# Performance work log

Measured on AMD Instinct MI355X. Metric: run time of the kernel, lower is better.

## Reference

```python
import jax, jax.numpy as jnp
import numpy as np

EPS = 0.97  # ContrastLoss eps
T = 0.07    # temperature

def _embed(x, W, b):
    # Linear + L2 normalize (Normalize(power=2))
    h = x @ W.T + b                     # [B, feat_dim]
    norm = jnp.sqrt(jnp.sum(h * h, axis=1, keepdims=True))
    return h / norm

def setup_inputs() -> dict:
    key = jax.random.key(0)
    ks = jax.random.split(key, 7)
    B, S, Td, F = 8192, 2048, 2048, 128
    return {
        "f_s": jax.random.normal(ks[0], (B, S), jnp.float32),
        "f_t": jax.random.normal(ks[1], (B, Td), jnp.float32),
        "y": jax.random.randint(ks[2], (B,), 0, 100, jnp.int64),
        "W_s": jax.random.normal(ks[3], (F, S), jnp.float32) * 0.02,
        "b_s": jax.random.normal(ks[4], (F,), jnp.float32) * 0.02,
        "W_t": jax.random.normal(ks[5], (F, Td), jnp.float32) * 0.02,
        "b_t": jax.random.normal(ks[6], (F,), jnp.float32) * 0.02,
    }

def reference(f_s, f_t, y, W_s, b_s, W_t, b_t):
    fs = _embed(f_s, W_s, b_s)
    ft = _embed(f_t, W_t, b_t)
    # CRDLoss re-normalizes (idempotent, kept for fidelity)
    fs = fs / jnp.linalg.norm(fs, axis=1, keepdims=True)
    ft = ft / jnp.linalg.norm(ft, axis=1, keepdims=True)
    bsz = fs.shape[0]
    x = jnp.exp((fs @ ft.T) / T)  # [B, B] exponentiated similarities
    same = y[None, :] == y[:, None]        # y_expand == y_expand.T
    diag = jnp.eye(bsz, dtype=bool)
    pos_mask = same & ~diag
    neg_mask = ~same & ~diag
    # masked log-ratio sums instead of dynamic-shape gathers
    log_D1 = jnp.log(x / (x + EPS))
    log_D0 = jnp.log(EPS / (x + EPS))
    loss = -(jnp.sum(jnp.where(pos_mask, log_D1, 0.0))
             + jnp.sum(jnp.where(neg_mask, log_D0, 0.0))) / bsz
    return loss
```

## Files before the change

kernel.cpp:

```cpp
#include <hip/hip_runtime.h>
#include <math.h>


typedef _Float16 half_t;
typedef half_t halfx4 __attribute__((ext_vector_type(4)));
typedef half_t halfx8 __attribute__((ext_vector_type(8)));
typedef float f32x4 __attribute__((ext_vector_type(4)));

#define B_TOT   8192
#define K_EMB   2048
#define F_DIM   128
#define INV_T   14.285714285714286f
#define EPS_C   0.97f
#define CU_L2   20.60992915555662f
#define LN2_D   0.6931471805599453
#define LNEPS_D (-0.030459207484708574)

__device__ __forceinline__ float fexp2(float x) {
#if __has_builtin(__builtin_amdgcn_exp2f)
    return __builtin_amdgcn_exp2f(x);
#else
    return __expf(x * 0.6931471805599453f);
#endif
}
__device__ __forceinline__ float flog2(float x) {
#if __has_builtin(__builtin_amdgcn_logf)
    return __builtin_amdgcn_logf(x);
#else
    return __logf(x) * 1.4426950408889634f;
#endif
}

__global__ __launch_bounds__(256) void cvt_w_kernel(
    const float* __restrict__ Ws, const float* __restrict__ Wt,
    half_t* __restrict__ Ws16, half_t* __restrict__ Wt16)
{
    const float* src = blockIdx.y ? Wt : Ws;
    half_t* dst = blockIdx.y ? Wt16 : Ws16;
    int pos4 = blockIdx.x * 256 + threadIdx.x;
    float4 v = *(const float4*)(src + (size_t)pos4 * 4);
    halfx4 h4 = {(half_t)v.x, (half_t)v.y, (half_t)v.z, (half_t)v.w};
    *(halfx4*)(dst + (size_t)pos4 * 4) = h4;
}

__device__ __forceinline__ void cvst(uint4* dst, float4 x, float4 y)
{
    halfx8 h = {(half_t)x.x, (half_t)x.y, (half_t)x.z, (half_t)x.w,
                (half_t)y.x, (half_t)y.y, (half_t)y.z, (half_t)y.w};
    *(halfx8*)dst = h;
}

__device__ __forceinline__ void gload_lds16(const void* g, void* l)
{
    __builtin_amdgcn_global_load_lds(
        (const __attribute__((address_space(1))) void*)g,
        (__attribute__((address_space(3))) void*)l,
        16, 0, 0);
}

__global__ __launch_bounds__(256) void embed_kernel(
    const float* __restrict__ Xs, const float* __restrict__ Xt,
    const half_t* __restrict__ Ws16, const half_t* __restrict__ Wt16,
    const float* __restrict__ bs, const float* __restrict__ bt,
    half_t* __restrict__ outs, half_t* __restrict__ outt)
{
    const float* X; const half_t* W16; const float* bias; half_t* out;
    if (blockIdx.y == 0) { X = Xs; W16 = Ws16; bias = bs; out = outs; }
    else                 { X = Xt; W16 = Wt16; bias = bt; out = outt; }

    __shared__ uint4 smem[5120];

    const int tid  = threadIdx.x;
    const int r0   = blockIdx.x * 32;
    const int lane = tid & 63;
    const int w    = tid >> 6;
    const int wm   = w & 1, wn = w >> 1;
    const int l16  = lane & 15, lhi = lane >> 4;

    float bv[4];
#pragma unroll
    for (int in = 0; in < 4; ++in) bv[in] = bias[wn * 64 + in * 16 + l16];

    const int ar0 = tid >> 4;
    const int ac  = tid & 15;
    const int axz = ac ^ ar0;
    const float* aptr0 = X + (size_t)(r0 + ar0) * K_EMB + ac * 8;
    const float* aptr1 = aptr0 + (size_t)16 * K_EMB;

    const half_t* bgp[8];
#pragma unroll
    for (int i = 0; i < 8; ++i) {
        int rl = w * 32 + i * 4 + (lane >> 4);
        bgp[i] = W16 + (size_t)rl * K_EMB + (size_t)(((lane & 15) ^ (rl & 15)) * 8);
    }

    f32x4 acc[4];
#pragma unroll
    for (int in = 0; in < 4; ++in) acc[in] = f32x4{0.f, 0.f, 0.f, 0.f};

    float4 aR[4];

#define LOADA(T) do {                                                          \
        aR[0] = *(const float4*)(aptr0 + (size_t)(T) * 128);                   \
        aR[1] = *(const float4*)(aptr0 + (size_t)(T) * 128 + 4);               \
        aR[2] = *(const float4*)(aptr1 + (size_t)(T) * 128);                   \
        aR[3] = *(const float4*)(aptr1 + (size_t)(T) * 128 + 4);               \
    } while (0)

#define CVTA(BUF) do {                                                         \
        cvst(&smem[(BUF) * 512 + ar0 * 16 + axz], aR[0], aR[1]);               \
        cvst(&smem[(BUF) * 512 + ar0 * 16 + 256 + axz], aR[2], aR[3]);         \
    } while (0)

#define BGLL(BUF, T) do {                                                      \
        _Pragma("unroll")                                                      \
        for (int i = 0; i < 8; ++i)                                            \
            gload_lds16(bgp[i] + (size_t)(T) * 128,                            \
                        &smem[1024 + (BUF) * 2048 + w * 512 + i * 64]);        \
    } while (0)

#define COMPUTE(BUF) do {                                                      \
        _Pragma("unroll")                                                      \
        for (int kk = 0; kk < 4; ++kk) {                                       \
            const int sl = (kk * 4 + lhi) ^ l16;                               \
            halfx8 afrag = *(const halfx8*)&smem[(BUF) * 512 +                 \
                                                 (wm * 16 + l16) * 16 + sl];   \
            _Pragma("unroll")                                                  \
            for (int in = 0; in < 4; ++in) {                                   \
                halfx8 bfrag = *(const halfx8*)&smem[1024 + (BUF) * 2048 +     \
                                     (wn * 64 + in * 16 + l16) * 16 + sl];     \
                acc[in] = __builtin_amdgcn_mfma_f32_16x16x32_f16(              \
                    afrag, bfrag, acc[in], 0, 0, 0);                           \
            }                                                                  \
        }                                                                      \
    } while (0)

    BGLL(0, 0);
    LOADA(0);
    CVTA(0);
    LOADA(1);
    BGLL(1, 1);
    asm volatile("s_waitcnt lgkmcnt(0)" ::: "memory");
    __builtin_amdgcn_s_barrier();

#pragma unroll 2
    for (int t = 0; t < 14; ++t) {
        const int buf = t & 1;
        COMPUTE(buf);
        CVTA(buf ^ 1);
        LOADA(t + 2);
        asm volatile("s_waitcnt vmcnt(4) lgkmcnt(0)" ::: "memory");
        __builtin_amdgcn_s_barrier();
        BGLL(buf, t + 2);
    }
    COMPUTE(0);
    CVTA(1);
    asm volatile("s_waitcnt vmcnt(0) lgkmcnt(0)" ::: "memory");
    __builtin_amdgcn_s_barrier();
    COMPUTE(1);

#undef LOADA
#undef CVTA
#undef BGLL
#undef COMPUTE

    float* redS = (float*)smem;
    float* invS = ((float*)smem) + 64;

    float hh[4][4];
    float psum[4];
#pragma unroll
    for (int reg = 0; reg < 4; ++reg) {
        float p = 0.f;
#pragma unroll
        for (int in = 0; in < 4; ++in) {
            float v = acc[in][reg] + bv[in];
            hh[in][reg] = v;
            p += v * v;
        }
        p += __shfl_xor(p, 1);
        p += __shfl_xor(p, 2);
        p += __shfl_xor(p, 4);
        p += __shfl_xor(p, 8);
        psum[reg] = p;
    }
    if (l16 == 0)
#pragma unroll
        for (int reg = 0; reg < 4; ++reg)
            redS[(wm * 16 + lhi * 4 + reg) * 2 + wn] = psum[reg];
    __syncthreads();
    if (tid < 32) invS[tid] = rsqrtf(redS[tid * 2] + redS[tid * 2 + 1]);
    __syncthreads();

#pragma unroll
    for (int in = 0; in < 4; ++in)
#pragma unroll
        for (int reg = 0; reg < 4; ++reg) {
            int row = wm * 16 + lhi * 4 + reg;
            int col = wn * 64 + in * 16 + l16;
            out[(size_t)(r0 + row) * F_DIM + col] = (half_t)(hh[in][reg] * invS[row]);
        }
}

__global__ __launch_bounds__(256) void loss_kernel(
    const half_t* __restrict__ FS, const half_t* __restrict__ FT,
    const int* __restrict__ y, double* __restrict__ partials)
{
    __shared__ uint4 As4[128 * 8];
    __shared__ uint4 Bs4[128 * 8];
    __shared__ int   yrl[128], ycl[128];
    __shared__ float wsum[4];

    const int tid = threadIdx.x;
    const int i0  = blockIdx.x * 128;
    const int j0  = blockIdx.y * 128;

    if (tid < 128) yrl[tid] = y[i0 + tid];
    else           ycl[tid - 128] = y[j0 + tid - 128];

    const int lane = tid & 63;
    const int w    = tid >> 6;
    const int wm   = w >> 1, wn = w & 1;
    const int l16  = lane & 15, lhi = lane >> 4;

#pragma unroll
    for (int i = 0; i < 4; ++i) {
        int f = tid + i * 256;
        int row = f >> 3, c = f & 7;
        As4[row * 8 + (c ^ (row & 7))] = *(const uint4*)(FS + (size_t)(i0 + row) * F_DIM + c * 8);
    }
#pragma unroll
    for (int i = 0; i < 4; ++i) {
        int f = tid + i * 256;
        int row = f >> 3, c = f & 7;
        Bs4[row * 8 + (c ^ (row & 7))] = *(const uint4*)(FT + (size_t)(j0 + row) * F_DIM + c * 8);
    }
    __syncthreads();

    f32x4 acc[4][4];
    for (int im = 0; im < 4; ++im)
        for (int in = 0; in < 4; ++in)
            acc[im][in] = f32x4{0.f, 0.f, 0.f, 0.f};

    for (int kc = 0; kc < 2; ++kc) {
#pragma unroll
        for (int kk = 0; kk < 2; ++kk) {
            halfx8 a[4], b[4];
#pragma unroll
            for (int im = 0; im < 4; ++im) {
                int r = wm * 64 + im * 16 + l16;
                a[im] = *(const halfx8*)&As4[r * 8 + ((kk * 4 + lhi) ^ (r & 7))];
            }
#pragma unroll
            for (int in = 0; in < 4; ++in) {
                int r = wn * 64 + in * 16 + l16;
                b[in] = *(const halfx8*)&Bs4[r * 8 + ((kk * 4 + lhi) ^ (r & 7))];
            }
#pragma unroll
            for (int im = 0; im < 4; ++im)
#pragma unroll
                for (int in = 0; in < 4; ++in)
                    acc[im][in] = __builtin_amdgcn_mfma_f32_16x16x32_f16(
                        a[im], b[in], acc[im][in], 0, 0, 0);
        }
        if (kc == 0) {
            __syncthreads();
#pragma unroll
            for (int i = 0; i < 4; ++i) {
                int f = tid + i * 256;
                int row = f >> 3, c = f & 7;
                As4[row * 8 + (c ^ (row & 7))] =
                    *(const uint4*)(FS + (size_t)(i0 + row) * F_DIM + 64 + c * 8);
            }
#pragma unroll
            for (int i = 0; i < 4; ++i) {
                int f = tid + i * 256;
                int row = f >> 3, c = f & 7;
                Bs4[row * 8 + (c ^ (row & 7))] =
                    *(const uint4*)(FT + (size_t)(j0 + row) * F_DIM + 64 + c * 8);
            }
            __syncthreads();
        }
    }

    int yclv[4];
#pragma unroll
    for (int in = 0; in < 4; ++in) yclv[in] = ycl[wn * 64 + in * 16 + l16];

    float sumL = 0.f, sumU = 0.f;
    if (i0 != j0) {
#pragma unroll
        for (int im = 0; im < 4; ++im)
#pragma unroll
            for (int reg = 0; reg < 4; ++reg) {
                const int yi = yrl[wm * 64 + im * 16 + lhi * 4 + reg];
#pragma unroll
                for (int in = 0; in < 4; ++in) {
                    float u  = acc[im][in][reg] * CU_L2;
                    float e  = fexp2(u);
                    float l2 = flog2(e + EPS_C);
                    sumL += l2;
                    sumU += (yi == yclv[in]) ? u : 0.f;
                }
            }
    } else {
#pragma unroll
        for (int im = 0; im < 4; ++im)
#pragma unroll
            for (int reg = 0; reg < 4; ++reg) {
                const int il = wm * 64 + im * 16 + lhi * 4 + reg;
                const int yi = yrl[il];
#pragma unroll
                for (int in = 0; in < 4; ++in) {
                    const int jl = wn * 64 + in * 16 + l16;
                    float u  = acc[im][in][reg] * CU_L2;
                    float e  = fexp2(u);
                    float l2 = flog2(e + EPS_C);
                    bool off = (il != jl);
                    sumL += off ? l2 : 0.f;
                    sumU += (off && yi == yclv[in]) ? u : 0.f;
                }
            }
    }

    float local = sumU - sumL;
    for (int m = 1; m < 64; m <<= 1) local += __shfl_xor(local, m);
    if (lane == 0) wsum[w] = local;
    __syncthreads();
    if (tid == 0)
        partials[blockIdx.y * gridDim.x + blockIdx.x] =
            ((double)wsum[0] + (double)wsum[1]) + ((double)wsum[2] + (double)wsum[3]);
}

__global__ __launch_bounds__(256) void finalize_kernel(
    const double* __restrict__ partials, const int* __restrict__ y,
    float* __restrict__ out)
{
    __shared__ double sh[4];
    __shared__ int hist[128];
    if (threadIdx.x < 128) hist[threadIdx.x] = 0;
    __syncthreads();
    for (int i = threadIdx.x; i < B_TOT; i += 256) atomicAdd(&hist[y[i]], 1);

    double loc = 0.0;
    for (int i = threadIdx.x; i < 4096; i += 256) loc += partials[i];
    for (int m = 1; m < 64; m <<= 1) loc += __shfl_xor(loc, m);
    int lane = threadIdx.x & 63, w = threadIdx.x >> 6;
    if (lane == 0) sh[w] = loc;
    __syncthreads();
    if (threadIdx.x == 0) {
        long long npos = 0;
        for (int c = 0; c < 128; ++c) {
            long long n = hist[c];
            npos += n * n;
        }
        npos -= B_TOT;
        long long nneg = (long long)B_TOT * (B_TOT - 1) - npos;
        double total = (sh[0] + sh[1]) + (sh[2] + sh[3]);
        out[0] = (float)(-(LN2_D * total + (double)nneg * LNEPS_D) / (double)B_TOT);
    }
}

extern "C" void kernel_launch(void* const* d_in, const int* in_sizes, int n_in,
                              void* d_out, int out_size, void* d_ws, size_t ws_size,
                              hipStream_t stream)
{
    const size_t WS_NEEDED = (64 << 10) + (4 << 20) + (1 << 20);
    if (ws_size < WS_NEEDED) return;

    const float* f_s = (const float*)d_in[0];
    const float* f_t = (const float*)d_in[1];
    const int*   y   = (const int*)d_in[2];
    const float* W_s = (const float*)d_in[3];
    const float* b_s = (const float*)d_in[4];
    const float* W_t = (const float*)d_in[5];
    const float* b_t = (const float*)d_in[6];
    float* out = (float*)d_out;

    char* ws = (char*)d_ws;
    double* partials = (double*)ws;
    half_t* fs   = (half_t*)(ws + (64 << 10));
    half_t* ft   = (half_t*)(ws + (64 << 10) + (2 << 20));
    half_t* Ws16 = (half_t*)(ws + (64 << 10) + (4 << 20));
    half_t* Wt16 = (half_t*)(ws + (64 << 10) + (4 << 20) + (512 << 10));

    cvt_w_kernel<<<dim3(256, 2), 256, 0, stream>>>(W_s, W_t, Ws16, Wt16);
    embed_kernel<<<dim3(256, 2), 256, 0, stream>>>(f_s, f_t, Ws16, Wt16, b_s, b_t, fs, ft);
    loss_kernel<<<dim3(64, 64), 256, 0, stream>>>(fs, ft, y, partials);
    finalize_kernel<<<1, 256, 0, stream>>>(partials, y, out);
    (void)in_sizes; (void)n_in; (void)out_size;
}
```

Measured before the change: 207.9 us.

## Rewrite embed GEMM to load operands straight into registers without LDS

The embed kernel drops the LDS double-buffered staging, with its async global-to-LDS loads for W and the converted A tiles. Each wave now loads its A rows and W fragments directly from global memory into registers, converts A to fp16 in registers, and software-pipelines two k-steps. Blocks grow to 512 threads (8 waves, each covering 16 rows by 32 columns) so there is more parallelism to hide load latency. The aim is to cut LDS traffic and barriers in a memory-bound projection, at the cost of more redundant global/L2 reads of W across waves and less coalesced access.

After: 276.7 us. 33.1% more time.

```diff
diff --git a/kernel.cpp b/kernel.cpp
--- a/kernel.cpp
+++ b/kernel.cpp
@@ -43,22 +43,7 @@
     *(halfx4*)(dst + (size_t)pos4 * 4) = h4;
 }
 
-__device__ __forceinline__ void cvst(uint4* dst, float4 x, float4 y)
-{
-    halfx8 h = {(half_t)x.x, (half_t)x.y, (half_t)x.z, (half_t)x.w,
-                (half_t)y.x, (half_t)y.y, (half_t)y.z, (half_t)y.w};
-    *(halfx8*)dst = h;
-}
-
-__device__ __forceinline__ void gload_lds16(const void* g, void* l)
-{
-    __builtin_amdgcn_global_load_lds(
-        (const __attribute__((address_space(1))) void*)g,
-        (__attribute__((address_space(3))) void*)l,
-        16, 0, 0);
-}
-
-__global__ __launch_bounds__(256) void embed_kernel(
+__global__ __launch_bounds__(512, 4) void embed_kernel(
     const float* __restrict__ Xs, const float* __restrict__ Xt,
     const half_t* __restrict__ Ws16, const half_t* __restrict__ Wt16,
     const float* __restrict__ bs, const float* __restrict__ bt,
@@ -68,116 +53,75 @@
     if (blockIdx.y == 0) { X = Xs; W16 = Ws16; bias = bs; out = outs; }
     else                 { X = Xt; W16 = Wt16; bias = bt; out = outt; }
 
-    __shared__ uint4 smem[5120];
+    __shared__ float redS[32][4];
+    __shared__ float invS[32];
 
     const int tid  = threadIdx.x;
     const int r0   = blockIdx.x * 32;
     const int lane = tid & 63;
     const int w    = tid >> 6;
-    const int wm   = w & 1, wn = w >> 1;
+    const int wr   = w & 1;
+    const int wc   = w >> 1;
     const int l16  = lane & 15, lhi = lane >> 4;
 
-    float bv[4];
-#pragma unroll
-    for (int in = 0; in < 4; ++in) bv[in] = bias[wn * 64 + in * 16 + l16];
-
-    const int ar0 = tid >> 4;
-    const int ac  = tid & 15;
-    const int axz = ac ^ ar0;
-    const float* aptr0 = X + (size_t)(r0 + ar0) * K_EMB + ac * 8;
-    const float* aptr1 = aptr0 + (size_t)16 * K_EMB;
-
-    const half_t* bgp[8];
-#pragma unroll
-    for (int i = 0; i < 8; ++i) {
-        int rl = w * 32 + i * 4 + (lane >> 4);
-        bgp[i] = W16 + (size_t)rl * K_EMB + (size_t)(((lane & 15) ^ (rl & 15)) * 8);
-    }
-
-    f32x4 acc[4];
-#pragma unroll
-    for (int in = 0; in < 4; ++in) acc[in] = f32x4{0.f, 0.f, 0.f, 0.f};
-
-    float4 aR[4];
-
-#define LOADA(T) do {                                                          \
-        aR[0] = *(const float4*)(aptr0 + (size_t)(T) * 128);                   \
-        aR[1] = *(const float4*)(aptr0 + (size_t)(T) * 128 + 4);               \
-        aR[2] = *(const float4*)(aptr1 + (size_t)(T) * 128);                   \
-        aR[3] = *(const float4*)(aptr1 + (size_t)(T) * 128 + 4);               \
+    float bv0 = bias[wc * 32 + l16];
+    float bv1 = bias[wc * 32 + 16 + l16];
+
+    const float* ap = X + (size_t)(r0 + wr * 16 + l16) * K_EMB + lhi * 8;
+    const half_t* bp0 = W16 + (size_t)(wc * 32 + l16) * K_EMB + lhi * 8;
+    const half_t* bp1 = bp0 + (size_t)16 * K_EMB;
+
+    f32x4 acc0 = f32x4{0.f, 0.f, 0.f, 0.f};
+    f32x4 acc1 = f32x4{0.f, 0.f, 0.f, 0.f};
+
+#define LOADT(a0, a1, a2, a3, b00, b01, b10, b11, T) do {                      \
+        a0  = *(const float4*)(ap + (size_t)(T) * 64);                         \
+        a1  = *(const float4*)(ap + (size_t)(T) * 64 + 4);                     \
+        a2  = *(const float4*)(ap + (size_t)(T) * 64 + 32);                    \
+        a3  = *(const float4*)(ap + (size_t)(T) * 64 + 36);                    \
+        b00 = *(const halfx8*)(bp0 + (size_t)(T) * 64);                        \
+        b01 = *(const halfx8*)(bp0 + (size_t)(T) * 64 + 32);                   \
+        b10 = *(const halfx8*)(bp1 + (size_t)(T) * 64);                        \
+        b11 = *(const halfx8*)(bp1 + (size_t)(T) * 64 + 32);                   \
     } while (0)
 
-#define CVTA(BUF) do {                                                         \
-        cvst(&smem[(BUF) * 512 + ar0 * 16 + axz], aR[0], aR[1]);               \
-        cvst(&smem[(BUF) * 512 + ar0 * 16 + 256 + axz], aR[2], aR[3]);         \
+#define COMPT(a0, a1, a2, a3, b00, b01, b10, b11) do {                         \
+        halfx8 af0 = {(half_t)a0.x, (half_t)a0.y, (half_t)a0.z, (half_t)a0.w, \
+                      (half_t)a1.x, (half_t)a1.y, (half_t)a1.z, (half_t)a1.w};\
+        halfx8 af1 = {(half_t)a2.x, (half_t)a2.y, (half_t)a2.z, (half_t)a2.w, \
+                      (half_t)a3.x, (half_t)a3.y, (half_t)a3.z, (half_t)a3.w};\
+        acc0 = __builtin_amdgcn_mfma_f32_16x16x32_f16(af0, b00, acc0, 0, 0, 0);\
+        acc1 = __builtin_amdgcn_mfma_f32_16x16x32_f16(af0, b10, acc1, 0, 0, 0);\
+        acc0 = __builtin_amdgcn_mfma_f32_16x16x32_f16(af1, b01, acc0, 0, 0, 0);\
+        acc1 = __builtin_amdgcn_mfma_f32_16x16x32_f16(af1, b11, acc1, 0, 0, 0);\
     } while (0)
 
-#define BGLL(BUF, T) do {                                                      \
-        _Pragma("unroll")                                                      \
-        for (int i = 0; i < 8; ++i)                                            \
-            gload_lds16(bgp[i] + (size_t)(T) * 128,                            \
-                        &smem[1024 + (BUF) * 2048 + w * 512 + i * 64]);        \
-    } while (0)
-
-#define COMPUTE(BUF) do {                                                      \
-        _Pragma("unroll")                                                      \
-        for (int kk = 0; kk < 4; ++kk) {                                       \
-            const int sl = (kk * 4 + lhi) ^ l16;                               \
-            halfx8 afrag = *(const halfx8*)&smem[(BUF) * 512 +                 \
-                                                 (wm * 16 + l16) * 16 + sl];   \
-            _Pragma("unroll")                                                  \
-            for (int in = 0; in < 4; ++in) {                                   \
-                halfx8 bfrag = *(const halfx8*)&smem[1024 + (BUF) * 2048 +     \
-                                     (wn * 64 + in * 16 + l16) * 16 + sl];     \
-                acc[in] = __builtin_amdgcn_mfma_f32_16x16x32_f16(              \
-                    afrag, bfrag, acc[in], 0, 0, 0);                           \
-            }                                                                  \
-        }                                                                      \
-    } while (0)
-
-    BGLL(0, 0);
-    LOADA(0);
-    CVTA(0);
-    LOADA(1);
-    BGLL(1, 1);
-    asm volatile("s_waitcnt lgkmcnt(0)" ::: "memory");
-    __builtin_amdgcn_s_barrier();
-
-#pragma unroll 2
-    for (int t = 0; t < 14; ++t) {
-        const int buf = t & 1;
-        COMPUTE(buf);
-        CVTA(buf ^ 1);
-        LOADA(t + 2);
-        asm volatile("s_waitcnt vmcnt(4) lgkmcnt(0)" ::: "memory");
-        __builtin_amdgcn_s_barrier();
-        BGLL(buf, t + 2);
-    }
-    COMPUTE(0);
-    CVTA(1);
-    asm volatile("s_waitcnt vmcnt(0) lgkmcnt(0)" ::: "memory");
-    __builtin_amdgcn_s_barrier();
-    COMPUTE(1);
-
-#undef LOADA
-#undef CVTA
-#undef BGLL
-#undef COMPUTE
-
-    float* redS = (float*)smem;
-    float* invS = ((float*)smem) + 64;
-
-    float hh[4][4];
+    float4 xa0, xa1, xa2, xa3; halfx8 yb00, yb01, yb10, yb11;
+    float4 za0, za1, za2, za3; halfx8 wb00, wb01, wb10, wb11;
+
+    LOADT(xa0, xa1, xa2, xa3, yb00, yb01, yb10, yb11, 0);
+#pragma unroll 1
+    for (int t = 0; t < 30; t += 2) {
+        LOADT(za0, za1, za2, za3, wb00, wb01, wb10, wb11, t + 1);
+        COMPT(xa0, xa1, xa2, xa3, yb00, yb01, yb10, yb11);
+        LOADT(xa0, xa1, xa2, xa3, yb00, yb01, yb10, yb11, t + 2);
+        COMPT(za0, za1, za2, za3, wb00, wb01, wb10, wb11);
+    }
+    LOADT(za0, za1, za2, za3, wb00, wb01, wb10, wb11, 31);
+    COMPT(xa0, xa1, xa2, xa3, yb00, yb01, yb10, yb11);
+    COMPT(za0, za1, za2, za3, wb00, wb01, wb10, wb11);
+
+#undef LOADT
+#undef COMPT
+
+    float h0[4], h1[4];
     float psum[4];
 #pragma unroll
     for (int reg = 0; reg < 4; ++reg) {
-        float p = 0.f;
-#pragma unroll
-        for (int in = 0; in < 4; ++in) {
-            float v = acc[in][reg] + bv[in];
-            hh[in][reg] = v;
-            p += v * v;
-        }
+        float v0 = acc0[reg] + bv0;
+        float v1 = acc1[reg] + bv1;
+        h0[reg] = v0; h1[reg] = v1;
+        float p = v0 * v0 + v1 * v1;
         p += __shfl_xor(p, 1);
         p += __shfl_xor(p, 2);
         p += __shfl_xor(p, 4);
@@ -187,19 +131,20 @@
     if (l16 == 0)
 #pragma unroll
         for (int reg = 0; reg < 4; ++reg)
-            redS[(wm * 16 + lhi * 4 + reg) * 2 + wn] = psum[reg];
-    __syncthreads();
-    if (tid < 32) invS[tid] = rsqrtf(redS[tid * 2] + redS[tid * 2 + 1]);
-    __syncthreads();
-
-#pragma unroll
-    for (int in = 0; in < 4; ++in)
-#pragma unroll
-        for (int reg = 0; reg < 4; ++reg) {
-            int row = wm * 16 + lhi * 4 + reg;
-            int col = wn * 64 + in * 16 + l16;
-            out[(size_t)(r0 + row) * F_DIM + col] = (half_t)(hh[in][reg] * invS[row]);
-        }
+            redS[wr * 16 + lhi * 4 + reg][wc] = psum[reg];
+    __syncthreads();
+    if (tid < 32)
+        invS[tid] = rsqrtf((redS[tid][0] + redS[tid][1]) +
+                           (redS[tid][2] + redS[tid][3]));
+    __syncthreads();
+
+#pragma unroll
+    for (int reg = 0; reg < 4; ++reg) {
+        int row = wr * 16 + lhi * 4 + reg;
+        float s = invS[row];
+        out[(size_t)(r0 + row) * F_DIM + wc * 32 + l16]      = (half_t)(h0[reg] * s);
+        out[(size_t)(r0 + row) * F_DIM + wc * 32 + 16 + l16] = (half_t)(h1[reg] * s);
+    }
 }
 
 __global__ __launch_bounds__(256) void loss_kernel(
@@ -385,7 +330,7 @@
     half_t* Wt16 = (half_t*)(ws + (64 << 10) + (4 << 20) + (512 << 10));
 
     cvt_w_kernel<<<dim3(256, 2), 256, 0, stream>>>(W_s, W_t, Ws16, Wt16);
-    embed_kernel<<<dim3(256, 2), 256, 0, stream>>>(f_s, f_t, Ws16, Wt16, b_s, b_t, fs, ft);
+    embed_kernel<<<dim3(256, 2), 512, 0, stream>>>(f_s, f_t, Ws16, Wt16, b_s, b_t, fs, ft);
     loss_kernel<<<dim3(64, 64), 256, 0, stream>>>(fs, ft, y, partials);
     finalize_kernel<<<1, 256, 0, stream>>>(partials, y, out);
     (void)in_sizes; (void)n_in; (void)out_size;
```
